# Optimization experiments

Hardware: AMD Instinct MI355X
Metric: run time of the kernel (lower is better)

The kernel has to match this reference:

```python
import jax, jax.numpy as jnp
import numpy as np

N, D, N_CLASSES = 8192, 512, 128
POS_MARGIN = 1.0  # default path: sample_method=None, Dynamic_margin=None


def setup_inputs() -> dict:
    key = jax.random.key(0)
    k1, k2 = jax.random.split(key)
    x = jax.random.normal(k1, (N, D), dtype=jnp.float32)
    # metric-learning embeddings are L2-normalized so sim in [-1, 1]
    x = x / jnp.linalg.norm(x, axis=1, keepdims=True)
    targets = jax.random.randint(k2, (N,), 0, N_CLASSES, dtype=jnp.int64)
    return {"inputs": x, "targets": targets, "nonorm": 0}


def reference(inputs, targets, nonorm):
    n = inputs.shape[0]
    sim = jnp.matmul(inputs, inputs.T)                      # [n, n]
    same = targets[:, None] == targets[None, :]             # [n, n]
    pos_mask = same & (sim < POS_MARGIN)                    # drops self-sim == 1
    neg_mask = ~same

    # per-row masked log-sum-exp (sort in original is irrelevant to the sums)
    pos_sum = jnp.sum(jnp.where(pos_mask, jnp.exp(1.0 - sim), 0.0), axis=1)
    neg_sum = jnp.sum(jnp.where(neg_mask, jnp.exp(sim), 0.0), axis=1)
    pos_loss = jnp.log(pos_sum)
    neg_loss = jnp.log(neg_sum)

    has_neg = jnp.any(neg_mask, axis=1)                     # rows w/o negs are skipped
    loss = jnp.sum(jnp.where(has_neg, pos_loss + neg_loss, 0.0)) / n
    prec = jnp.mean(1.0 - has_neg.astype(jnp.float32))      # fraction of skipped rows

    # torch code reports means of the LAST row's pos/neg pairs
    last_pos = pos_mask[-1]
    last_neg = neg_mask[-1]
    mean_pos_sim = jnp.sum(jnp.where(last_pos, sim[-1], 0.0)) / jnp.sum(last_pos)
    mean_neg_sim = jnp.sum(jnp.where(last_neg, sim[-1], 0.0)) / jnp.sum(last_neg)
    return loss, prec, mean_pos_sim, mean_neg_sim
```

## Files before the change

kernel.cpp:

```cpp
#include <hip/hip_runtime.h>
#include <math.h>

#define N_ 8192
#define D_ 512
#define NC_ 128
#define T_ 64

typedef __attribute__((ext_vector_type(8))) short bf16x8;
typedef __attribute__((ext_vector_type(4))) float f32x4;
typedef __attribute__((ext_vector_type(4))) unsigned short us4;

static __device__ __forceinline__ unsigned short f2bf(float f) {
    union { float f; unsigned u; } c; c.f = f;
    unsigned u = c.u;
    u += 0x7fffu + ((u >> 16) & 1u);
    return (unsigned short)(u >> 16);
}

__global__ __launch_bounds__(256) void k_convert(const float* __restrict__ x,
                                                 unsigned short* __restrict__ xb) {
    int i = (blockIdx.x * 256 + threadIdx.x);
    float4 v = reinterpret_cast<const float4*>(x)[i];
    us4 o = { f2bf(v.x), f2bf(v.y), f2bf(v.z), f2bf(v.w) };
    reinterpret_cast<us4*>(xb)[i] = o;
}

__global__ __launch_bounds__(512, 4) void k_main(const unsigned short* __restrict__ xb,
                                                 const int* __restrict__ tg,
                                                 float* __restrict__ bufP,
                                                 float* __restrict__ bufN) {
    __shared__ alignas(16) unsigned short As[128 * 64];
    __shared__ alignas(16) unsigned short Bs[256 * 64];
    __shared__ int rowT[128];

    const int tid  = threadIdx.x;
    const int w    = tid >> 6;
    const int lane = tid & 63;
    const int q    = lane >> 4;
    const int l15  = lane & 15;
    const int wrow = w >> 2;
    const int wcol = w & 3;

    int rem = blockIdx.x;
    int it = 0;
    while (rem >= 32 - (it >> 1)) { rem -= 32 - (it >> 1); it++; }
    const int jt2  = (it >> 1) + rem;
    const int row0 = it * 128;
    const int col0 = jt2 * 256;

    const int bsub   = 2 * jt2 + (wcol >> 1);
    const bool rowOK = (bsub >= it);

    if (tid < 128) rowT[tid] = tg[row0 + tid];
    __syncthreads();

    int tR[4][4];
#pragma unroll
    for (int mi = 0; mi < 4; ++mi)
#pragma unroll
        for (int r = 0; r < 4; ++r)
            tR[mi][r] = rowT[wrow * 64 + mi * 16 + q * 4 + r];

    int tC[4];
#pragma unroll
    for (int ni = 0; ni < 4; ++ni)
        tC[ni] = tg[col0 + wcol * 64 + ni * 16 + l15];

    f32x4 acc[4][4];
#pragma unroll
    for (int mi = 0; mi < 4; ++mi)
#pragma unroll
        for (int ni = 0; ni < 4; ++ni)
            acc[mi][ni] = (f32x4){0.f, 0.f, 0.f, 0.f};

    for (int ks = 0; ks < 8; ++ks) {
        const int k0 = ks * 64;
        __syncthreads();
#pragma unroll
        for (int i2 = 0; i2 < 2; ++i2) {
            int slot = i2 * 512 + tid;
            int r  = slot >> 3;
            int s  = slot & 7;
            int g  = s ^ (r & 7);
            const unsigned short* ga = xb + (size_t)(row0 + r) * D_ + k0 + g * 8;
            __builtin_amdgcn_global_load_lds(
                (const __attribute__((address_space(1))) void*)ga,
                (__attribute__((address_space(3))) void*)(As + (i2 * 512 + w * 64) * 8),
                16, 0, 0);
        }
#pragma unroll
        for (int i2 = 0; i2 < 4; ++i2) {
            int slot = i2 * 512 + tid;
            int r  = slot >> 3;
            int s  = slot & 7;
            int g  = s ^ (r & 7);
            const unsigned short* gb = xb + (size_t)(col0 + r) * D_ + k0 + g * 8;
            __builtin_amdgcn_global_load_lds(
                (const __attribute__((address_space(1))) void*)gb,
                (__attribute__((address_space(3))) void*)(Bs + (i2 * 512 + w * 64) * 8),
                16, 0, 0);
        }
        __syncthreads();

#pragma unroll
        for (int kc = 0; kc < 2; ++kc) {
            bf16x8 aF[4], bF[4];
#pragma unroll
            for (int mi = 0; mi < 4; ++mi) {
                int rA = wrow * 64 + mi * 16 + l15;
                int g  = kc * 4 + q;
                int s  = g ^ (rA & 7);
                aF[mi] = *reinterpret_cast<const bf16x8*>(As + rA * 64 + s * 8);
            }
#pragma unroll
            for (int ni = 0; ni < 4; ++ni) {
                int rB = wcol * 64 + ni * 16 + l15;
                int g  = kc * 4 + q;
                int s  = g ^ (rB & 7);
                bF[ni] = *reinterpret_cast<const bf16x8*>(Bs + rB * 64 + s * 8);
            }
#pragma unroll
            for (int mi = 0; mi < 4; ++mi)
#pragma unroll
                for (int ni = 0; ni < 4; ++ni)
                    acc[mi][ni] = __builtin_amdgcn_mfma_f32_16x16x32_bf16(
                        aF[mi], bF[ni], acc[mi][ni], 0, 0, 0);
        }
    }

    float ps[4][4], ns[4][4];
    float cps[4], cns[4];
#pragma unroll
    for (int mi = 0; mi < 4; ++mi)
#pragma unroll
        for (int r = 0; r < 4; ++r) { ps[mi][r] = 0.f; ns[mi][r] = 0.f; }
#pragma unroll
    for (int ni = 0; ni < 4; ++ni) { cps[ni] = 0.f; cns[ni] = 0.f; }

    if (rowOK) {
#pragma unroll
        for (int mi = 0; mi < 4; ++mi)
#pragma unroll
            for (int ni = 0; ni < 4; ++ni)
#pragma unroll
                for (int r = 0; r < 4; ++r) {
                    float s = acc[mi][ni][r];
                    bool same = (tR[mi][r] == tC[ni]);
                    float e = __expf(same ? 1.0f - s : s);
                    float pe = (same && (s < 1.0f)) ? e : 0.0f;
                    float ne = same ? 0.0f : e;
                    ps[mi][r] += pe; ns[mi][r] += ne;
                    cps[ni]   += pe; cns[ni]   += ne;
                }
    }

    __syncthreads();
    float* scr = (float*)As;

#pragma unroll
    for (int mi = 0; mi < 4; ++mi)
#pragma unroll
        for (int r = 0; r < 4; ++r) {
            float p = ps[mi][r];
            float n = ns[mi][r];
#pragma unroll
            for (int m = 1; m < 16; m <<= 1) {
                p += __shfl_xor(p, m, 64);
                n += __shfl_xor(n, m, 64);
            }
            if (l15 == 0) {
                int rloc = wrow * 64 + mi * 16 + q * 4 + r;
                scr[wcol * 128 + rloc]       = p;
                scr[512 + wcol * 128 + rloc] = n;
            }
        }

#pragma unroll
    for (int ni = 0; ni < 4; ++ni) {
        float p = cps[ni];
        float n = cns[ni];
        p += __shfl_xor(p, 16, 64); p += __shfl_xor(p, 32, 64);
        n += __shfl_xor(n, 16, 64); n += __shfl_xor(n, 32, 64);
        if (q == 0) {
            int cloc = wcol * 64 + ni * 16 + l15;
            scr[1024 + wrow * 256 + cloc] = p;
            scr[1536 + wrow * 256 + cloc] = n;
        }
    }
    __syncthreads();

    if (tid < 128) {
        int r = tid;
        int s_row = it + jt2 - (it >> 1);
        size_t off = ((size_t)it * T_ + s_row) * 128 + r;
        bufP[off] = scr[r] + scr[128 + r] + scr[256 + r] + scr[384 + r];
        bufN[off] = scr[512 + r] + scr[640 + r] + scr[768 + r] + scr[896 + r];
    } else if (tid < 384) {
        int c  = tid - 128;
        int bc = 2 * jt2 + (c >> 7);
        if (bc > it) {
            size_t off = ((size_t)bc * T_ + it) * 128 + (c & 127);
            bufP[off] = scr[1024 + c] + scr[1280 + c];
            bufN[off] = scr[1536 + c] + scr[1792 + c];
        }
    }
}

__global__ __launch_bounds__(256) void k_last(const float* __restrict__ x,
                                              double* __restrict__ sim_last) {
    int j    = (blockIdx.x * 256 + threadIdx.x) >> 6;
    int lane = threadIdx.x & 63;
    const float* xl = x + (size_t)(N_ - 1) * D_;
    const float* xj = x + (size_t)j * D_;
    double acc = 0.0;
#pragma unroll
    for (int it = 0; it < 8; ++it) {
        int k = it * 64 + lane;
        acc += (double)xl[k] * (double)xj[k];
    }
#pragma unroll
    for (int m = 32; m >= 1; m >>= 1) acc += __shfl_xor(acc, m, 64);
    if (lane == 0) sim_last[j] = acc;
}

__global__ __launch_bounds__(256) void k_reduce(const float* __restrict__ bufP,
                                                const float* __restrict__ bufN,
                                                float* __restrict__ psum,
                                                float* __restrict__ nsum) {
    int t    = blockIdx.x;
    int half = threadIdx.x >> 7;
    int r    = threadIdx.x & 127;
    int smax = t + 32 - (t >> 1);
    const float* buf = half ? bufN : bufP;
    const float* base = buf + (size_t)t * T_ * 128 + r;
    float s = 0.f;
    for (int o = 0; o < smax; ++o) s += base[o * 128];
    if (half) nsum[t * 128 + r] = s;
    else      psum[t * 128 + r] = s;
}

__global__ __launch_bounds__(1024) void k_final(const float* __restrict__ psum,
                                                const float* __restrict__ nsum,
                                                const int* __restrict__ tg,
                                                const double* __restrict__ sim_last,
                                                float* __restrict__ out) {
    __shared__ int lh[NC_];
    __shared__ double sl[1024], sp[1024], sn[1024];
    __shared__ int    sk[1024], cp[1024], cn[1024];
    int tid = threadIdx.x;

    if (tid < NC_) lh[tid] = 0;
    __syncthreads();
    for (int i = tid; i < N_; i += 1024) atomicAdd(&lh[tg[i]], 1);
    __syncthreads();

    double part = 0.0;
    int skip = 0;
    for (int i = tid; i < N_; i += 1024) {
        if (lh[tg[i]] < N_) {
            part += (double)(logf(psum[i]) + logf(nsum[i]));
        } else {
            skip++;
        }
    }

    double pd = 0.0, nd = 0.0;
    int pc = 0, nc = 0;
    int tlast = tg[N_ - 1];
    for (int j = tid; j < N_; j += 1024) {
        double s = sim_last[j];
        if (tg[j] == tlast) {
            if (s < 1.0) { pd += s; pc++; }
        } else {
            nd += s; nc++;
        }
    }

    sl[tid] = part; sk[tid] = skip;
    sp[tid] = pd;   cp[tid] = pc;
    sn[tid] = nd;   cn[tid] = nc;
    __syncthreads();
    for (int s = 512; s >= 1; s >>= 1) {
        if (tid < s) {
            sl[tid] += sl[tid + s]; sk[tid] += sk[tid + s];
            sp[tid] += sp[tid + s]; cp[tid] += cp[tid + s];
            sn[tid] += sn[tid + s]; cn[tid] += cn[tid + s];
        }
        __syncthreads();
    }
    if (tid == 0) {
        out[0] = (float)(sl[0] / (double)N_);
        out[1] = (float)sk[0] / (float)N_;
        out[2] = (float)(sp[0] / (double)cp[0]);
        out[3] = (float)(sn[0] / (double)cn[0]);
    }
}

extern "C" void kernel_launch(void* const* d_in, const int* in_sizes, int n_in,
                              void* d_out, int out_size, void* d_ws, size_t ws_size,
                              hipStream_t stream) {
    const float* x  = (const float*)d_in[0];
    const int*   tg = (const int*)d_in[1];
    char* ws = (char*)d_ws;

    unsigned short* xb = (unsigned short*)ws;
    const size_t XB = (size_t)N_ * D_ * 2;
    float*  psum     = (float*)(ws + XB);
    float*  nsum     = (float*)(ws + XB + 32768);
    double* sim_last = (double*)(ws + XB + 65536);
    float*  bufP     = (float*)(ws + XB + 131072);
    float*  bufN     = (float*)(ws + XB + 131072 + 2097152);

    const int nblk = 1056;

    hipLaunchKernelGGL(k_convert, dim3((N_ * D_) / (256 * 4)), dim3(256), 0, stream, x, xb);
    hipLaunchKernelGGL(k_main, dim3(nblk), dim3(512), 0, stream, xb, tg, bufP, bufN);
    hipLaunchKernelGGL(k_last, dim3((N_ * 64) / 256), dim3(256), 0, stream, x, sim_last);
    hipLaunchKernelGGL(k_reduce, dim3(T_), dim3(256), 0, stream, bufP, bufN, psum, nsum);
    hipLaunchKernelGGL(k_final, dim3(1), dim3(1024), 0, stream,
                       psum, nsum, tg, sim_last, (float*)d_out);
}
```

Measured before the change: 167.0 us.

## Fuse small kernels into prep and tail passes with last-block finalize

Folds the bf16 conversion, the last-row similarity dot products and the class histogram into a single prep kernel. The per-tile row reduction and the final scalar reduction are merged into one tail kernel that accumulates with atomics and lets the last finishing block compute the outputs. This cuts the launch count from five to three and removes the single-block final kernel's serial loop over all rows. In exchange it adds atomic counters, fences and a double-precision atomicAdd, and the summation order now depends on block completion order.

```diff
diff --git a/kernel.cpp b/kernel.cpp
--- a/kernel.cpp
+++ b/kernel.cpp
@@ -17,12 +17,43 @@
     return (unsigned short)(u >> 16);
 }
 
-__global__ __launch_bounds__(256) void k_convert(const float* __restrict__ x,
-                                                 unsigned short* __restrict__ xb) {
-    int i = (blockIdx.x * 256 + threadIdx.x);
-    float4 v = reinterpret_cast<const float4*>(x)[i];
-    us4 o = { f2bf(v.x), f2bf(v.y), f2bf(v.z), f2bf(v.w) };
-    reinterpret_cast<us4*>(xb)[i] = o;
+__global__ __launch_bounds__(256) void k_prep(const float* __restrict__ x,
+                                              const int* __restrict__ tg,
+                                              unsigned short* __restrict__ xb,
+                                              double* __restrict__ sim_last,
+                                              int* __restrict__ hist,
+                                              int* __restrict__ done,
+                                              int* __restrict__ skipAcc,
+                                              double* __restrict__ lossAcc) {
+    const int b = blockIdx.x;
+    if (b < 4096) {
+        int i = b * 256 + threadIdx.x;
+        float4 v = reinterpret_cast<const float4*>(x)[i];
+        us4 o = { f2bf(v.x), f2bf(v.y), f2bf(v.z), f2bf(v.w) };
+        reinterpret_cast<us4*>(xb)[i] = o;
+    } else if (b < 6144) {
+        int j    = ((b - 4096) * 256 + threadIdx.x) >> 6;
+        int lane = threadIdx.x & 63;
+        const float* xl = x + (size_t)(N_ - 1) * D_;
+        const float* xj = x + (size_t)j * D_;
+        double acc = 0.0;
+#pragma unroll
+        for (int it = 0; it < 8; ++it) {
+            int k = it * 64 + lane;
+            acc += (double)xl[k] * (double)xj[k];
+        }
+#pragma unroll
+        for (int m = 32; m >= 1; m >>= 1) acc += __shfl_xor(acc, m, 64);
+        if (lane == 0) sim_last[j] = acc;
+    } else {
+        __shared__ int lh[NC_];
+        if (threadIdx.x < NC_) lh[threadIdx.x] = 0;
+        if (threadIdx.x == 0) { *done = 0; *skipAcc = 0; *lossAcc = 0.0; }
+        __syncthreads();
+        for (int i = threadIdx.x; i < N_; i += 256) atomicAdd(&lh[tg[i]], 1);
+        __syncthreads();
+        if (threadIdx.x < NC_) hist[threadIdx.x] = lh[threadIdx.x];
+    }
 }
 
 __global__ __launch_bounds__(512, 4) void k_main(const unsigned short* __restrict__ xb,
@@ -206,93 +237,89 @@
     }
 }
 
-__global__ __launch_bounds__(256) void k_last(const float* __restrict__ x,
-                                              double* __restrict__ sim_last) {
-    int j    = (blockIdx.x * 256 + threadIdx.x) >> 6;
-    int lane = threadIdx.x & 63;
-    const float* xl = x + (size_t)(N_ - 1) * D_;
-    const float* xj = x + (size_t)j * D_;
-    double acc = 0.0;
-#pragma unroll
-    for (int it = 0; it < 8; ++it) {
-        int k = it * 64 + lane;
-        acc += (double)xl[k] * (double)xj[k];
-    }
-#pragma unroll
-    for (int m = 32; m >= 1; m >>= 1) acc += __shfl_xor(acc, m, 64);
-    if (lane == 0) sim_last[j] = acc;
-}
-
-__global__ __launch_bounds__(256) void k_reduce(const float* __restrict__ bufP,
-                                                const float* __restrict__ bufN,
-                                                float* __restrict__ psum,
-                                                float* __restrict__ nsum) {
-    int t    = blockIdx.x;
-    int half = threadIdx.x >> 7;
-    int r    = threadIdx.x & 127;
-    int smax = t + 32 - (t >> 1);
-    const float* buf = half ? bufN : bufP;
+__global__ __launch_bounds__(256) void k_tail(const float* __restrict__ bufP,
+                                              const float* __restrict__ bufN,
+                                              const int* __restrict__ tg,
+                                              const int* __restrict__ hist,
+                                              const double* __restrict__ sim_last,
+                                              int* __restrict__ done,
+                                              int* __restrict__ skipAcc,
+                                              double* __restrict__ lossAcc,
+                                              float* __restrict__ out) {
+    __shared__ float  pn[256];
+    __shared__ double sdA[256], sdB[256];
+    __shared__ int    siA[256], siB[256];
+    __shared__ int    amLast;
+
+    const int tid  = threadIdx.x;
+    const int t    = blockIdx.x;
+    const int half = tid >> 7;
+    const int r    = tid & 127;
+    const int smax = t + 32 - (t >> 1);
+
+    const float* buf  = half ? bufN : bufP;
     const float* base = buf + (size_t)t * T_ * 128 + r;
     float s = 0.f;
     for (int o = 0; o < smax; ++o) s += base[o * 128];
-    if (half) nsum[t * 128 + r] = s;
-    else      psum[t * 128 + r] = s;
-}
-
-__global__ __launch_bounds__(1024) void k_final(const float* __restrict__ psum,
-                                                const float* __restrict__ nsum,
-                                                const int* __restrict__ tg,
-                                                const double* __restrict__ sim_last,
-                                                float* __restrict__ out) {
-    __shared__ int lh[NC_];
-    __shared__ double sl[1024], sp[1024], sn[1024];
-    __shared__ int    sk[1024], cp[1024], cn[1024];
-    int tid = threadIdx.x;
-
-    if (tid < NC_) lh[tid] = 0;
-    __syncthreads();
-    for (int i = tid; i < N_; i += 1024) atomicAdd(&lh[tg[i]], 1);
+    pn[tid] = s;
     __syncthreads();
 
     double part = 0.0;
     int skip = 0;
-    for (int i = tid; i < N_; i += 1024) {
-        if (lh[tg[i]] < N_) {
-            part += (double)(logf(psum[i]) + logf(nsum[i]));
-        } else {
-            skip++;
-        }
+    if (half == 0) {
+        int gi = t * 128 + r;
+        if (hist[tg[gi]] < N_) part = (double)(logf(pn[r]) + logf(pn[128 + r]));
+        else skip = 1;
+    }
+    sdA[tid] = part; siA[tid] = skip;
+    __syncthreads();
+    for (int st = 128; st >= 1; st >>= 1) {
+        if (tid < st) { sdA[tid] += sdA[tid + st]; siA[tid] += siA[tid + st]; }
+        __syncthreads();
+    }
+
+    if (tid == 0) {
+        atomicAdd(lossAcc, sdA[0]);
+        atomicAdd(skipAcc, siA[0]);
+        __threadfence();
+        amLast = (atomicAdd(done, 1) == T_ - 1);
+    }
+    __syncthreads();
+    if (!amLast) return;
+
+    __shared__ double finLoss;
+    __shared__ int    finSkip;
+    if (tid == 0) {
+        __threadfence();
+        finLoss = atomicAdd(lossAcc, 0.0);
+        finSkip = atomicAdd(skipAcc, 0);
     }
 
     double pd = 0.0, nd = 0.0;
     int pc = 0, nc = 0;
     int tlast = tg[N_ - 1];
-    for (int j = tid; j < N_; j += 1024) {
-        double s = sim_last[j];
+    for (int j = tid; j < N_; j += 256) {
+        double sv = sim_last[j];
         if (tg[j] == tlast) {
-            if (s < 1.0) { pd += s; pc++; }
+            if (sv < 1.0) { pd += sv; pc++; }
         } else {
-            nd += s; nc++;
-        }
-    }
-
-    sl[tid] = part; sk[tid] = skip;
-    sp[tid] = pd;   cp[tid] = pc;
-    sn[tid] = nd;   cn[tid] = nc;
-    __syncthreads();
-    for (int s = 512; s >= 1; s >>= 1) {
-        if (tid < s) {
-            sl[tid] += sl[tid + s]; sk[tid] += sk[tid + s];
-            sp[tid] += sp[tid + s]; cp[tid] += cp[tid + s];
-            sn[tid] += sn[tid + s]; cn[tid] += cn[tid + s];
+            nd += sv; nc++;
+        }
+    }
+    sdA[tid] = pd; sdB[tid] = nd; siA[tid] = pc; siB[tid] = nc;
+    __syncthreads();
+    for (int st = 128; st >= 1; st >>= 1) {
+        if (tid < st) {
+            sdA[tid] += sdA[tid + st]; sdB[tid] += sdB[tid + st];
+            siA[tid] += siA[tid + st]; siB[tid] += siB[tid + st];
         }
         __syncthreads();
     }
     if (tid == 0) {
-        out[0] = (float)(sl[0] / (double)N_);
-        out[1] = (float)sk[0] / (float)N_;
-        out[2] = (float)(sp[0] / (double)cp[0]);
-        out[3] = (float)(sn[0] / (double)cn[0]);
+        out[0] = (float)(finLoss / (double)N_);
+        out[1] = (float)finSkip / (float)N_;
+        out[2] = (float)(sdA[0] / (double)siA[0]);
+        out[3] = (float)(sdB[0] / (double)siB[0]);
     }
 }
 
@@ -305,18 +332,21 @@
 
     unsigned short* xb = (unsigned short*)ws;
     const size_t XB = (size_t)N_ * D_ * 2;
-    float*  psum     = (float*)(ws + XB);
-    float*  nsum     = (float*)(ws + XB + 32768);
-    double* sim_last = (double*)(ws + XB + 65536);
-    float*  bufP     = (float*)(ws + XB + 131072);
-    float*  bufN     = (float*)(ws + XB + 131072 + 2097152);
+    double* sim_last = (double*)(ws + XB);
+    float*  bufP     = (float*)(ws + XB + 65536);
+    float*  bufN     = (float*)(ws + XB + 65536 + 2097152);
+    char*   ctrl     = ws + XB + 65536 + 2 * 2097152;
+    int*    hist     = (int*)ctrl;
+    int*    done     = (int*)(ctrl + 512);
+    int*    skipAcc  = (int*)(ctrl + 516);
+    double* lossAcc  = (double*)(ctrl + 520);
 
     const int nblk = 1056;
 
-    hipLaunchKernelGGL(k_convert, dim3((N_ * D_) / (256 * 4)), dim3(256), 0, stream, x, xb);
+    hipLaunchKernelGGL(k_prep, dim3(4096 + 2048 + 1), dim3(256), 0, stream,
+                       x, tg, xb, sim_last, hist, done, skipAcc, lossAcc);
     hipLaunchKernelGGL(k_main, dim3(nblk), dim3(512), 0, stream, xb, tg, bufP, bufN);
-    hipLaunchKernelGGL(k_last, dim3((N_ * 64) / 256), dim3(256), 0, stream, x, sim_last);
-    hipLaunchKernelGGL(k_reduce, dim3(T_), dim3(256), 0, stream, bufP, bufN, psum, nsum);
-    hipLaunchKernelGGL(k_final, dim3(1), dim3(1024), 0, stream,
-                       psum, nsum, tg, sim_last, (float*)d_out);
-}
+    hipLaunchKernelGGL(k_tail, dim3(T_), dim3(256), 0, stream,
+                       bufP, bufN, tg, hist, sim_last, done, skipAcc, lossAcc,
+                       (float*)d_out);
+}
```

Measured after the change: 173.1 us. 3.7% more time.
